# Performance work log

Measured on AMD Instinct MI355X. Metric: run time of the kernel, lower is better.

## Reference

```python
import jax, jax.numpy as jnp
import numpy as np

N_FFT = 2048
HOP = 512
PAD = N_FFT // 2  # 1024, center padding
FREQ_BINS = N_FFT // 2 + 1  # 1025


def _fourier_kernels():
    # freq_scale='no', window='hann' (fftbins=True): w[n] = 0.5 - 0.5*cos(2*pi*n/N)
    s = np.arange(N_FFT, dtype=np.float64)
    win = 0.5 - 0.5 * np.cos(2.0 * np.pi * s / N_FFT)
    k = np.arange(FREQ_BINS, dtype=np.float64)[:, None]
    phase = 2.0 * np.pi * k * s[None, :] / N_FFT  # (freq_bins, n_fft)
    wsin = (win[None, :] * np.sin(phase)).astype(np.float32)
    wcos = (win[None, :] * np.cos(phase)).astype(np.float32)
    return wcos, wsin


def setup_inputs() -> dict:
    key = jax.random.key(0)
    x = jax.random.normal(key, (32, 220500), dtype=jnp.float32)
    wcos, wsin = _fourier_kernels()
    return {"x": x, "wcos": jnp.asarray(wcos), "wsin": jnp.asarray(wsin)}


def reference(x, wcos, wsin):
    # x: (B, L). center=True, pad_mode='reflect'
    xp = jnp.pad(x, ((0, 0), (PAD, PAD)), mode="reflect")[:, None, :]  # (B,1,Lp)
    dn = ("NCH", "OIH", "NCH")
    # one conv with both bases stacked -> (B, 2*freq_bins, T)
    kern = jnp.concatenate([wcos, wsin], axis=0)[:, None, :]  # (2F,1,n_fft)
    spec = jax.lax.conv_general_dilated(
        xp, kern, window_strides=(HOP,), padding="VALID", dimension_numbers=dn
    )
    real, imag = spec[:, :FREQ_BINS, :], spec[:, FREQ_BINS:, :]
    # output_format='Complex': stack (real, -imag) on last axis
    return jnp.stack([real, -imag], axis=-1)  # (B, F, T, 2)
```

## Files before the change

### kernel.cpp

```cpp
#include <hip/hip_runtime.h>
#include <hip/hip_bf16.h>

#define L_IN   220500
#define PADK   1024
#define LP     222548
#define LPP    222560
#define BATCH  32
#define HOPSZ  512
#define T_FR   431
#define F_BINS 1025
#define M_TOT  (BATCH * T_FR)
#define N_GEMM 2048
#define K_TOT  2048
#define NT_K   32

typedef short short8 __attribute__((ext_vector_type(8)));
typedef float floatx4 __attribute__((ext_vector_type(4)));

__device__ __forceinline__ void glds16(const void* g, void* l) {
    __builtin_amdgcn_global_load_lds(
        (const __attribute__((address_space(1))) void*)g,
        (__attribute__((address_space(3))) void*)l, 16, 0, 0);
}

__device__ __forceinline__ short f2bf(float f) {
    __hip_bfloat16 h = __float2bfloat16(f);
    return *reinterpret_cast<short*>(&h);
}

__global__ void k_prep_x(const float* __restrict__ x, __hip_bfloat16* __restrict__ xp) {
    int c = blockIdx.x * 256 + threadIdx.x;
    int b = blockIdx.y;
    int i0 = c * 8;
    if (i0 >= LP) return;
    const float* xb = x + (size_t)b * L_IN;
    __hip_bfloat16* xpb = xp + (size_t)b * LPP;
    if (i0 >= PADK && i0 + 8 <= PADK + L_IN) {
        const float4* s4 = (const float4*)(xb + (i0 - PADK));
        float4 a = s4[0], d = s4[1];
        short8 o;
        o[0]=f2bf(a.x); o[1]=f2bf(a.y); o[2]=f2bf(a.z); o[3]=f2bf(a.w);
        o[4]=f2bf(d.x); o[5]=f2bf(d.y); o[6]=f2bf(d.z); o[7]=f2bf(d.w);
        *(short8*)((short*)xpb + i0) = o;
    } else {
        for (int u = 0; u < 8; ++u) {
            int i = i0 + u;
            if (i >= LP) break;
            int j = i - PADK;
            if (j < 0) j = -j;
            if (j >= L_IN) j = 2 * L_IN - 2 - j;
            xpb[i] = __float2bfloat16(xb[j]);
        }
    }
}

__global__ void k_prep_w(const float* __restrict__ wcos, const float* __restrict__ wsin,
                         __hip_bfloat16* __restrict__ wb) {
    int c = blockIdx.x * 256 + threadIdx.x;
    int i0 = c * 8;
    if (i0 >= N_GEMM * K_TOT) return;
    int np = i0 >> 11;
    int k  = i0 & (K_TOT - 1);
    int kf = np >> 1;
    const float* src = ((np & 1) ? wsin : wcos) + (size_t)kf * K_TOT + k;
    float4 a = ((const float4*)src)[0], d = ((const float4*)src)[1];
    short8 o;
    o[0]=f2bf(a.x); o[1]=f2bf(a.y); o[2]=f2bf(a.z); o[3]=f2bf(a.w);
    o[4]=f2bf(d.x); o[5]=f2bf(d.y); o[6]=f2bf(d.z); o[7]=f2bf(d.w);
    *(short8*)((short*)wb + i0) = o;
}

__global__ void k_nyq(const __hip_bfloat16* __restrict__ xp, const float* __restrict__ wcos,
                      float* __restrict__ out) {
    int f = blockIdx.x * 4 + (threadIdx.x >> 6);
    if (f >= M_TOT) return;
    int lane = threadIdx.x & 63;
    int b = f / T_FR, t = f - b * T_FR;
    const __hip_bfloat16* xr = xp + (size_t)b * LPP + t * HOPSZ;
    const float* wr = wcos + (size_t)1024 * K_TOT;
    float sum = 0.f;
    #pragma unroll
    for (int i = 0; i < 4; ++i) {
        int s = i * 512 + lane * 8;
        short8 xv = *(const short8*)((const short*)xr + s);
        const float4* wv = (const float4*)(wr + s);
        float4 w0 = wv[0], w1 = wv[1];
        float xs[8];
        #pragma unroll
        for (int u = 0; u < 8; ++u)
            xs[u] = __uint_as_float(((unsigned)(unsigned short)xv[u]) << 16);
        sum += xs[0]*w0.x + xs[1]*w0.y + xs[2]*w0.z + xs[3]*w0.w
             + xs[4]*w1.x + xs[5]*w1.y + xs[6]*w1.z + xs[7]*w1.w;
    }
    #pragma unroll
    for (int off = 32; off > 0; off >>= 1) sum += __shfl_xor(sum, off);
    if (lane == 0) {
        float2 v; v.x = sum; v.y = 0.f;
        ((float2*)out)[((size_t)b * F_BINS + 1024) * T_FR + t] = v;
    }
}

#define BARRIER { asm volatile("" ::: "memory"); __builtin_amdgcn_s_barrier(); asm volatile("" ::: "memory"); }
#define LGKM0   asm volatile("s_waitcnt lgkmcnt(0)" ::: "memory")
#define SP1     __builtin_amdgcn_s_setprio(1)
#define SP0     __builtin_amdgcn_s_setprio(0)

__global__ __launch_bounds__(512, 2) void k_gemm(
    const __hip_bfloat16* __restrict__ xp,
    const __hip_bfloat16* __restrict__ wb,
    float* __restrict__ out) {

    __shared__ short lds[65536];

    const int tid   = threadIdx.x;
    const int wave  = tid >> 6;
    const int lane  = tid & 63;
    const int quad  = lane >> 4;
    const int l15   = lane & 15;
    const int waveM = wave >> 2;
    const int waveN = wave & 3;

    const int bn = blockIdx.x & 7;
    const int bm = blockIdx.x >> 3;

    int arow[2][2], brow[2][2];
    #pragma unroll
    for (int h = 0; h < 2; ++h)
        #pragma unroll
        for (int q = 0; q < 2; ++q) {
            int m = bm * 256 + h * 128 + wave * 16 + q * 8 + (lane >> 3);
            if (m > M_TOT - 1) m = M_TOT - 1;
            int b = m / T_FR, t = m - b * T_FR;
            arow[h][q] = b * LPP + t * HOPSZ;
            int n = bn * 256 + h * 128 + wave * 16 + q * 8 + (lane >> 3);
            brow[h][q] = n * K_TOT;
        }
    const int colo = (((lane & 7) ^ (lane >> 3)) << 3);

#define STA(BUF,H,K0) { _Pragma("unroll") for (int q = 0; q < 2; ++q) \
        glds16(xp + arow[H][q] + (K0) + colo, &lds[((BUF)<<14) + ((H)<<13) + (wave*16 + q*8)*64]); }
#define STB(BUF,H,K0) { _Pragma("unroll") for (int q = 0; q < 2; ++q) \
        glds16(wb + brow[H][q] + (K0) + colo, &lds[32768 + ((BUF)<<14) + ((H)<<13) + (wave*16 + q*8)*64]); }
#define RDA(BUF,H) { _Pragma("unroll") for (int jm = 0; jm < 4; ++jm) { \
        int R = waveM*64 + jm*16 + l15; \
        _Pragma("unroll") for (int ks = 0; ks < 2; ++ks) \
            xf[jm][ks] = *(const short8*)&lds[((BUF)<<14) + ((H)<<13) + R*64 + (((ks*4+quad) ^ (R & 7)) << 3)]; } }
#define RDB(BUF,H,WF) { _Pragma("unroll") for (int jn = 0; jn < 2; ++jn) { \
        int R = waveN*32 + jn*16 + l15; \
        _Pragma("unroll") for (int ks = 0; ks < 2; ++ks) \
            WF[jn][ks] = *(const short8*)&lds[32768 + ((BUF)<<14) + ((H)<<13) + R*64 + (((ks*4+quad) ^ (R & 7)) << 3)]; } }
#define MFMA16(ACC, WF) { _Pragma("unroll") for (int jm = 0; jm < 4; ++jm) \
        _Pragma("unroll") for (int jn = 0; jn < 2; ++jn) \
        _Pragma("unroll") for (int ks = 0; ks < 2; ++ks) \
            ACC[jm][jn] = __builtin_amdgcn_mfma_f32_16x16x32_bf16(WF[jn][ks], xf[jm][ks], ACC[jm][jn], 0, 0, 0); }

    short8 xf[4][2], wf0[2][2], wf1[2][2];
    floatx4 a00[4][2] = {}, a01[4][2] = {}, a10[4][2] = {}, a11[4][2] = {};

    STA(0,0,0); STB(0,0,0); STB(0,1,0); STA(0,1,0);
    STA(1,0,64); STB(1,0,64); STB(1,1,64);
    asm volatile("s_waitcnt vmcnt(6)" ::: "memory");
    BARRIER;

#define TILE(T, BUF) { \
     \
    RDA(BUF, 0); RDB(BUF, 0, wf0); \
    if ((T) + 1 < NT_K) STA(BUF^1, 1, ((T)+1)*64); \
    BARRIER; LGKM0; SP1; MFMA16(a00, wf0); SP0; BARRIER; \
     \
    RDB(BUF, 1, wf1); \
    if ((T) + 2 < NT_K) STA(BUF, 0, ((T)+2)*64); \
    BARRIER; LGKM0; SP1; MFMA16(a01, wf1); SP0; BARRIER; \
     \
    RDA(BUF, 1); \
    if ((T) + 2 < NT_K) STB(BUF, 0, ((T)+2)*64); \
    BARRIER; LGKM0; SP1; MFMA16(a10, wf0); SP0; BARRIER; \
     \
    if ((T) + 2 < NT_K) STB(BUF, 1, ((T)+2)*64); \
    BARRIER; LGKM0; SP1; MFMA16(a11, wf1); SP0; \
    if ((T) == NT_K - 2) { asm volatile("s_waitcnt vmcnt(0)" ::: "memory"); } \
    else                 { asm volatile("s_waitcnt vmcnt(6)" ::: "memory"); } \
    BARRIER; \
}

    #pragma unroll 1
    for (int T = 0; T < NT_K; T += 2) {
        TILE(T, 0);
        TILE(T + 1, 1);
    }

    float2* __restrict__ out2 = (float2*)out;
#define EPI(ACC, QM, QN) { _Pragma("unroll") for (int jm = 0; jm < 4; ++jm) { \
        int m = bm*256 + QM*128 + waveM*64 + jm*16 + l15; \
        if (m < M_TOT) { \
            int b = m / T_FR, t = m - b * T_FR; \
            long tbase = (long)b * (F_BINS * T_FR) + t; \
            _Pragma("unroll") for (int jn = 0; jn < 2; ++jn) { \
                int nb = bn*256 + QN*128 + waveN*32 + jn*16 + quad*4; \
                _Pragma("unroll") for (int p = 0; p < 2; ++p) { \
                    int k = (nb + 2*p) >> 1; \
                    float2 v; v.x = ACC[jm][jn][2*p]; v.y = -ACC[jm][jn][2*p+1]; \
                    out2[tbase + (long)k * T_FR] = v; \
                } } } } }
    EPI(a00, 0, 0); EPI(a01, 0, 1); EPI(a10, 1, 0); EPI(a11, 1, 1);
}

extern "C" void kernel_launch(void* const* d_in, const int* in_sizes, int n_in,
                              void* d_out, int out_size, void* d_ws, size_t ws_size,
                              hipStream_t stream) {
    const float* x    = (const float*)d_in[0];
    const float* wcos = (const float*)d_in[1];
    const float* wsin = (const float*)d_in[2];
    float* out = (float*)d_out;

    __hip_bfloat16* xp = (__hip_bfloat16*)d_ws;
    __hip_bfloat16* wb = (__hip_bfloat16*)((char*)d_ws + (size_t)BATCH * LPP * sizeof(__hip_bfloat16));

    const int xchunks = (LP + 7) / 8;
    k_prep_x<<<dim3((xchunks + 255) / 256, BATCH), 256, 0, stream>>>(x, xp);
    k_prep_w<<<(N_GEMM * K_TOT / 8) / 256, 256, 0, stream>>>(wcos, wsin, wb);
    k_gemm<<<432, 512, 0, stream>>>(xp, wb, out);
    k_nyq<<<(M_TOT + 3) / 4, 256, 0, stream>>>(xp, wcos, out);
}
```

Baseline: 268.4 us.

## Software-pipeline LDS reads in GEMM and fuse prep and Nyquist kernels

Restructures the GEMM main loop so the LDS fragment reads for the next sub-tile are issued while the current MFMAs run. Explicit lgkmcnt waits and some barriers are removed, with sched_barriers added to keep ordering. The two prep kernels are merged into one launch, and the Nyquist-bin computation runs as extra blocks of the GEMM launch, filling idle CU slots and cutting launch overhead. This risks subtle LDS hazards if the waits or barrier placement are wrong.

Measured after the change: 259.6 us. 1.03x faster.

```diff
diff --git a/kernel.cpp b/kernel.cpp
--- a/kernel.cpp
+++ b/kernel.cpp
@@ -13,6 +13,10 @@
 #define N_GEMM 2048
 #define K_TOT  2048
 #define NT_K   32
+#define GEMM_BLOCKS 432
+#define NYQ_BLOCKS  48
+#define XBLOCKS 3488
+#define WBLOCKS 2048
 
 typedef short short8 __attribute__((ext_vector_type(8)));
 typedef float floatx4 __attribute__((ext_vector_type(4)));
@@ -28,86 +32,57 @@
     return *reinterpret_cast<short*>(&h);
 }
 
-__global__ void k_prep_x(const float* __restrict__ x, __hip_bfloat16* __restrict__ xp) {
-    int c = blockIdx.x * 256 + threadIdx.x;
-    int b = blockIdx.y;
-    int i0 = c * 8;
-    if (i0 >= LP) return;
-    const float* xb = x + (size_t)b * L_IN;
-    __hip_bfloat16* xpb = xp + (size_t)b * LPP;
-    if (i0 >= PADK && i0 + 8 <= PADK + L_IN) {
-        const float4* s4 = (const float4*)(xb + (i0 - PADK));
-        float4 a = s4[0], d = s4[1];
+__global__ void k_prep(const float* __restrict__ x,
+                       const float* __restrict__ wcos, const float* __restrict__ wsin,
+                       __hip_bfloat16* __restrict__ xp, __hip_bfloat16* __restrict__ wb) {
+    int blk = blockIdx.x;
+    if (blk < XBLOCKS) {
+        int b = blk / 109, ix = blk - b * 109;
+        int i0 = (ix * 256 + threadIdx.x) * 8;
+        if (i0 >= LP) return;
+        const float* xb = x + (size_t)b * L_IN;
+        __hip_bfloat16* xpb = xp + (size_t)b * LPP;
+        if (i0 >= PADK && i0 + 8 <= PADK + L_IN) {
+            const float4* s4 = (const float4*)(xb + (i0 - PADK));
+            float4 a = s4[0], d = s4[1];
+            short8 o;
+            o[0]=f2bf(a.x); o[1]=f2bf(a.y); o[2]=f2bf(a.z); o[3]=f2bf(a.w);
+            o[4]=f2bf(d.x); o[5]=f2bf(d.y); o[6]=f2bf(d.z); o[7]=f2bf(d.w);
+            *(short8*)((short*)xpb + i0) = o;
+        } else {
+            for (int u = 0; u < 8; ++u) {
+                int i = i0 + u;
+                if (i >= LP) break;
+                int j = i - PADK;
+                if (j < 0) j = -j;
+                if (j >= L_IN) j = 2 * L_IN - 2 - j;
+                xpb[i] = __float2bfloat16(xb[j]);
+            }
+        }
+    } else {
+        int i0 = ((blk - XBLOCKS) * 256 + threadIdx.x) * 8;
+        int np = i0 >> 11;
+        int k  = i0 & (K_TOT - 1);
+        int kf = np >> 1;
+        const float* src = ((np & 1) ? wsin : wcos) + (size_t)kf * K_TOT + k;
+        float4 a = ((const float4*)src)[0], d = ((const float4*)src)[1];
         short8 o;
         o[0]=f2bf(a.x); o[1]=f2bf(a.y); o[2]=f2bf(a.z); o[3]=f2bf(a.w);
         o[4]=f2bf(d.x); o[5]=f2bf(d.y); o[6]=f2bf(d.z); o[7]=f2bf(d.w);
-        *(short8*)((short*)xpb + i0) = o;
-    } else {
-        for (int u = 0; u < 8; ++u) {
-            int i = i0 + u;
-            if (i >= LP) break;
-            int j = i - PADK;
-            if (j < 0) j = -j;
-            if (j >= L_IN) j = 2 * L_IN - 2 - j;
-            xpb[i] = __float2bfloat16(xb[j]);
-        }
+        *(short8*)((short*)wb + i0) = o;
     }
 }
 
-__global__ void k_prep_w(const float* __restrict__ wcos, const float* __restrict__ wsin,
-                         __hip_bfloat16* __restrict__ wb) {
-    int c = blockIdx.x * 256 + threadIdx.x;
-    int i0 = c * 8;
-    if (i0 >= N_GEMM * K_TOT) return;
-    int np = i0 >> 11;
-    int k  = i0 & (K_TOT - 1);
-    int kf = np >> 1;
-    const float* src = ((np & 1) ? wsin : wcos) + (size_t)kf * K_TOT + k;
-    float4 a = ((const float4*)src)[0], d = ((const float4*)src)[1];
-    short8 o;
-    o[0]=f2bf(a.x); o[1]=f2bf(a.y); o[2]=f2bf(a.z); o[3]=f2bf(a.w);
-    o[4]=f2bf(d.x); o[5]=f2bf(d.y); o[6]=f2bf(d.z); o[7]=f2bf(d.w);
-    *(short8*)((short*)wb + i0) = o;
-}
-
-__global__ void k_nyq(const __hip_bfloat16* __restrict__ xp, const float* __restrict__ wcos,
-                      float* __restrict__ out) {
-    int f = blockIdx.x * 4 + (threadIdx.x >> 6);
-    if (f >= M_TOT) return;
-    int lane = threadIdx.x & 63;
-    int b = f / T_FR, t = f - b * T_FR;
-    const __hip_bfloat16* xr = xp + (size_t)b * LPP + t * HOPSZ;
-    const float* wr = wcos + (size_t)1024 * K_TOT;
-    float sum = 0.f;
-    #pragma unroll
-    for (int i = 0; i < 4; ++i) {
-        int s = i * 512 + lane * 8;
-        short8 xv = *(const short8*)((const short*)xr + s);
-        const float4* wv = (const float4*)(wr + s);
-        float4 w0 = wv[0], w1 = wv[1];
-        float xs[8];
-        #pragma unroll
-        for (int u = 0; u < 8; ++u)
-            xs[u] = __uint_as_float(((unsigned)(unsigned short)xv[u]) << 16);
-        sum += xs[0]*w0.x + xs[1]*w0.y + xs[2]*w0.z + xs[3]*w0.w
-             + xs[4]*w1.x + xs[5]*w1.y + xs[6]*w1.z + xs[7]*w1.w;
-    }
-    #pragma unroll
-    for (int off = 32; off > 0; off >>= 1) sum += __shfl_xor(sum, off);
-    if (lane == 0) {
-        float2 v; v.x = sum; v.y = 0.f;
-        ((float2*)out)[((size_t)b * F_BINS + 1024) * T_FR + t] = v;
-    }
-}
-
 #define BARRIER { asm volatile("" ::: "memory"); __builtin_amdgcn_s_barrier(); asm volatile("" ::: "memory"); }
-#define LGKM0   asm volatile("s_waitcnt lgkmcnt(0)" ::: "memory")
+#define VMW(N)  asm volatile("s_waitcnt vmcnt(" #N ")" ::: "memory")
+#define SCHED0  __builtin_amdgcn_sched_barrier(0)
 #define SP1     __builtin_amdgcn_s_setprio(1)
 #define SP0     __builtin_amdgcn_s_setprio(0)
 
 __global__ __launch_bounds__(512, 2) void k_gemm(
     const __hip_bfloat16* __restrict__ xp,
     const __hip_bfloat16* __restrict__ wb,
+    const float* __restrict__ wcos,
     float* __restrict__ out) {
 
     __shared__ short lds[65536];
@@ -115,6 +90,37 @@
     const int tid   = threadIdx.x;
     const int wave  = tid >> 6;
     const int lane  = tid & 63;
+
+    if (blockIdx.x >= GEMM_BLOCKS) {
+        const int gw = (blockIdx.x - GEMM_BLOCKS) * 8 + wave;
+        const float* wr = wcos + (size_t)1024 * K_TOT;
+        for (int f = gw; f < M_TOT; f += NYQ_BLOCKS * 8) {
+            int b = f / T_FR, t = f - b * T_FR;
+            const __hip_bfloat16* xr = xp + (size_t)b * LPP + t * HOPSZ;
+            float sum = 0.f;
+            #pragma unroll
+            for (int i = 0; i < 4; ++i) {
+                int s = i * 512 + lane * 8;
+                short8 xv = *(const short8*)((const short*)xr + s);
+                const float4* wv = (const float4*)(wr + s);
+                float4 w0 = wv[0], w1 = wv[1];
+                float xs[8];
+                #pragma unroll
+                for (int u = 0; u < 8; ++u)
+                    xs[u] = __uint_as_float(((unsigned)(unsigned short)xv[u]) << 16);
+                sum += xs[0]*w0.x + xs[1]*w0.y + xs[2]*w0.z + xs[3]*w0.w
+                     + xs[4]*w1.x + xs[5]*w1.y + xs[6]*w1.z + xs[7]*w1.w;
+            }
+            #pragma unroll
+            for (int off = 32; off > 0; off >>= 1) sum += __shfl_xor(sum, off);
+            if (lane == 0) {
+                float2 v; v.x = sum; v.y = 0.f;
+                ((float2*)out)[((size_t)b * F_BINS + 1024) * T_FR + t] = v;
+            }
+        }
+        return;
+    }
+
     const int quad  = lane >> 4;
     const int l15   = lane & 15;
     const int waveM = wave >> 2;
@@ -159,28 +165,37 @@
 
     STA(0,0,0); STB(0,0,0); STB(0,1,0); STA(0,1,0);
     STA(1,0,64); STB(1,0,64); STB(1,1,64);
-    asm volatile("s_waitcnt vmcnt(6)" ::: "memory");
+    VMW(6);
     BARRIER;
+    RDA(0,0); RDB(0,0,wf0);
 
 #define TILE(T, BUF) { \
      \
-    RDA(BUF, 0); RDB(BUF, 0, wf0); \
+    RDB(BUF, 1, wf1); \
     if ((T) + 1 < NT_K) STA(BUF^1, 1, ((T)+1)*64); \
-    BARRIER; LGKM0; SP1; MFMA16(a00, wf0); SP0; BARRIER; \
-     \
-    RDB(BUF, 1, wf1); \
+    SCHED0; \
+    SP1; MFMA16(a00, wf0); SP0; \
+    BARRIER; \
+     \
     if ((T) + 2 < NT_K) STA(BUF, 0, ((T)+2)*64); \
-    BARRIER; LGKM0; SP1; MFMA16(a01, wf1); SP0; BARRIER; \
-     \
+    SCHED0; \
+    SP1; MFMA16(a01, wf1); SP0; \
     RDA(BUF, 1); \
+    BARRIER; \
+     \
     if ((T) + 2 < NT_K) STB(BUF, 0, ((T)+2)*64); \
-    BARRIER; LGKM0; SP1; MFMA16(a10, wf0); SP0; BARRIER; \
-     \
+    SCHED0; \
+    SP1; MFMA16(a10, wf0); SP0; \
+    if ((T) + 1 < NT_K) { if ((T) < NT_K - 2) { VMW(8); } else { VMW(4); } } \
+    BARRIER; \
+     \
+    if ((T) + 1 < NT_K) RDB(BUF^1, 0, wf0); \
     if ((T) + 2 < NT_K) STB(BUF, 1, ((T)+2)*64); \
-    BARRIER; LGKM0; SP1; MFMA16(a11, wf1); SP0; \
-    if ((T) == NT_K - 2) { asm volatile("s_waitcnt vmcnt(0)" ::: "memory"); } \
-    else                 { asm volatile("s_waitcnt vmcnt(6)" ::: "memory"); } \
-    BARRIER; \
+    SCHED0; \
+    SP1; MFMA16(a11, wf1); SP0; \
+    if ((T) + 1 < NT_K) RDA(BUF^1, 0); \
+    if ((T) == NT_K - 2) { VMW(0); } else if ((T) < NT_K - 2) { VMW(6); } \
+    if ((T) + 1 < NT_K) BARRIER; \
 }
 
     #pragma unroll 1
@@ -216,9 +231,6 @@
     __hip_bfloat16* xp = (__hip_bfloat16*)d_ws;
     __hip_bfloat16* wb = (__hip_bfloat16*)((char*)d_ws + (size_t)BATCH * LPP * sizeof(__hip_bfloat16));
 
-    const int xchunks = (LP + 7) / 8;
-    k_prep_x<<<dim3((xchunks + 255) / 256, BATCH), 256, 0, stream>>>(x, xp);
-    k_prep_w<<<(N_GEMM * K_TOT / 8) / 256, 256, 0, stream>>>(wcos, wsin, wb);
-    k_gemm<<<432, 512, 0, stream>>>(xp, wb, out);
-    k_nyq<<<(M_TOT + 3) / 4, 256, 0, stream>>>(xp, wcos, out);
-}
+    k_prep<<<XBLOCKS + WBLOCKS, 256, 0, stream>>>(x, wcos, wsin, xp, wb);
+    k_gemm<<<GEMM_BLOCKS + NYQ_BLOCKS, 512, 0, stream>>>(xp, wb, wcos, out);
+}
```
